# Kernel tuning notes

Hardware: AMD Instinct MI355X
Metric: run time of the kernel (lower is better)

Reference implementation:

```python
import jax, jax.numpy as jnp
import numpy as np

N, E, R, D, S = 50000, 400000, 500, 128, 20
P = R * S
EPS = 1e-5

def setup_inputs() -> dict:
    key = jax.random.key(0)
    ks = jax.random.split(key, 20)
    xav = (2.0 / (D + D)) ** 0.5  # xavier_normal std for square layers
    def W(k):
        return jax.random.normal(k, (D, D), jnp.float32) * xav
    inp = {
        'ent_emb': jax.random.normal(ks[0], (N, D), jnp.float32),
        'rel_emb': jax.random.normal(ks[1], (R, D), jnp.float32),
        'edge_Wo': W(ks[2]), 'edge_bo': jnp.zeros((D,), jnp.float32),
        'edge_Wi': W(ks[3]), 'edge_bi': jnp.zeros((D,), jnp.float32),
        'edge_g': jnp.ones((D,), jnp.float32), 'edge_b': jnp.zeros((D,), jnp.float32),
        'node_Wo': W(ks[4]), 'node_bo': jnp.zeros((D,), jnp.float32),
        'node_Wi': W(ks[5]), 'node_bi': jnp.zeros((D,), jnp.float32),
        'node_g': jnp.ones((D,), jnp.float32), 'node_b': jnp.zeros((D,), jnp.float32),
        'comp_Wo': W(ks[6]), 'comp_bo': jnp.zeros((D,), jnp.float32),
        'comp_Wi': W(ks[7]), 'comp_bi': jnp.zeros((D,), jnp.float32),
        'comp_g': jnp.ones((D,), jnp.float32), 'comp_b': jnp.zeros((D,), jnp.float32),
        'relW': W(ks[8]), 'relb': jnp.zeros((D,), jnp.float32),
        'src': jax.random.randint(ks[9], (E,), 0, N),
        'dst': jax.random.randint(ks[10], (E,), 0, N),
        'etype': jax.random.randint(ks[11], (E,), 0, R),
        'heads': jax.random.randint(ks[13], (P,), 0, N),
        'tails': jax.random.randint(ks[14], (P,), 0, N),
        'rel_ids': jnp.repeat(jnp.arange(R), S),  # S sampled pairs per relation
    }
    in_mask = jax.random.randint(ks[12], (E,), 0, 2).astype(bool)
    inp['in_mask'] = in_mask
    inp['out_mask'] = ~in_mask  # DGL forward/reverse edge split: complementary masks
    return inp

def _edge_softmax(logit, dst, n):
    # segment softmax over edges grouped by destination node
    m = jax.ops.segment_max(logit, dst, num_segments=n)
    e = jnp.exp(logit - m[dst])
    s = jax.ops.segment_sum(e, dst, num_segments=n)
    return e / s[dst]

def _in_out(x, in_m, out_m, Wo, bo, Wi, bi):
    ho = x @ Wo.T + bo
    hi = x @ Wi.T + bi
    h = jnp.where(out_m[:, None], ho, jnp.zeros((), x.dtype))
    return jnp.where(in_m[:, None], hi, h)  # in-edges overwrite (masks disjoint)

def _bn_tanh(x, g, b):
    # training-mode BatchNorm1d (biased batch variance) + Tanh
    mu = jnp.mean(x, 0)
    var = jnp.mean(jnp.square(x - mu), 0)
    return jnp.tanh(g * (x - mu) * jax.lax.rsqrt(var + EPS) + b)

def reference(ent_emb, rel_emb,
              edge_Wo, edge_bo, edge_Wi, edge_bi, edge_g, edge_b,
              node_Wo, node_bo, node_Wi, node_bi, node_g, node_b,
              comp_Wo, comp_bo, comp_Wi, comp_bi, comp_g, comp_b,
              relW, relb,
              src, dst, etype, in_mask, out_mask, heads, tails, rel_ids):
    n = ent_emb.shape[0]
    r = rel_emb.shape[0]
    rel_e = rel_emb[etype]      # [E,D]
    e_src = ent_emb[src]        # [E,D]
    e_dst = ent_emb[dst]        # [E,D]

    # EdgeLayer: attn = e_dot_v(rel_e, dst_emb)
    a = _edge_softmax(jnp.sum(rel_e * e_dst, -1), dst, n)
    h = _in_out(rel_e, in_mask, out_mask, edge_Wo, edge_bo, edge_Wi, edge_bi) * a[:, None]
    edge_ent = _bn_tanh(jax.ops.segment_sum(h, dst, num_segments=n), edge_g, edge_b)

    # NodeLayer: attn = u_dot_v, message = src emb
    a = _edge_softmax(jnp.sum(e_src * e_dst, -1), dst, n)
    h = _in_out(e_src, in_mask, out_mask, node_Wo, node_bo, node_Wi, node_bi) * a[:, None]
    node_ent = _bn_tanh(jax.ops.segment_sum(h, dst, num_segments=n), node_g, node_b)

    # CompLayer (comp_fn='mul'): comp = u_mul_e, attn = e_dot_v(comp, dst)
    comp = e_src * rel_e
    a = _edge_softmax(jnp.sum(comp * e_dst, -1), dst, n)
    h = _in_out(comp, in_mask, out_mask, comp_Wo, comp_bo, comp_Wi, comp_bi) * a[:, None]
    comp_ent = _bn_tanh(jax.ops.segment_sum(h, dst, num_segments=n), comp_g, comp_b)

    final_ent = comp_ent + ent_emb + edge_ent + node_ent

    # update_relations: mean of w_rel_edge(tail - head) per relation
    pair = ent_emb[tails] - ent_emb[heads]          # [P,D]
    upd = pair @ relW.T + relb
    ssum = jax.ops.segment_sum(upd, rel_ids, num_segments=r)
    cnt = jax.ops.segment_sum(jnp.ones((rel_ids.shape[0],), jnp.float32), rel_ids, num_segments=r)
    cnt = jnp.maximum(cnt, 1.0)[:, None]
    final_rel = rel_emb + jnp.tanh(ssum / cnt)
    return final_ent, final_rel
```

## Files before the change

### kernel.cpp

```cpp
#include <hip/hip_runtime.h>
#include <stdint.h>

#define DN 128

typedef short s16x8 __attribute__((ext_vector_type(8)));
typedef float f32x4 __attribute__((ext_vector_type(4)));

__device__ __forceinline__ float bfs(unsigned short u){ return __uint_as_float(((uint32_t)u) << 16); }
__device__ __forceinline__ uint32_t f2bf(float f){
    uint32_t x = __float_as_uint(f);
    return (x + 0x7FFFu + ((x >> 16) & 1u)) >> 16;
}
__device__ __forceinline__ uint32_t packbf(float a, float b){ return f2bf(a) | (f2bf(b) << 16); }
__device__ __forceinline__ float tanh_(float x){
    float e = __expf(2.0f * x);
    return 1.0f - 2.0f / (e + 1.0f);
}

struct WC { const float* src[6]; };
__global__ void k_pre(const int* dst, int* counts,
                      const uint32_t* maskw, int nwords, int* flag,
                      WC wc, unsigned short* wcv, int E){
    int gid = blockIdx.x * 256 + threadIdx.x;
    if (gid < E) atomicAdd(&counts[dst[gid]], 1);
    if (gid < nwords && maskw[gid] > 1u) atomicOr(flag, 1);
    if (gid < 6 * 16384){
        int m = gid >> 14, o = gid & 16383;
        wcv[(size_t)m * 16384 + o] = (unsigned short)f2bf(wc.src[m][o]);
    }
}

__global__ void k_scan_a(const int* counts, int* bsums){
    int t = threadIdx.x;
    int s = counts[blockIdx.x * 256 + t];
    #pragma unroll
    for (int o = 32; o; o >>= 1) s += __shfl_xor(s, o);
    __shared__ int wsum[4];
    if ((t & 63) == 0) wsum[t >> 6] = s;
    __syncthreads();
    if (t == 0) bsums[blockIdx.x] = wsum[0] + wsum[1] + wsum[2] + wsum[3];
}

__global__ void k_scan_bc(const int* counts, const int* bsums, int nsb,
                          int* rowst, int* cursor, int npad, int E){
    __shared__ int pref;
    __shared__ int wsum[4];
    __shared__ int buf[256];
    int t = threadIdx.x, bid = blockIdx.x;
    int s = (t < bid && t < nsb) ? bsums[t] : 0;
    #pragma unroll
    for (int o = 32; o; o >>= 1) s += __shfl_xor(s, o);
    if ((t & 63) == 0) wsum[t >> 6] = s;
    __syncthreads();
    if (t == 0) pref = wsum[0] + wsum[1] + wsum[2] + wsum[3];
    int i = bid * 256 + t;
    int c = counts[i];
    buf[t] = c;
    __syncthreads();
    for (int o = 1; o < 256; o <<= 1){
        int add = (t >= o) ? buf[t - o] : 0;
        __syncthreads();
        buf[t] += add;
        __syncthreads();
    }
    int rsv = buf[t] - c + pref;
    rowst[i] = rsv; cursor[i] = rsv;
    if (i == npad - 1) rowst[npad] = E;
}

__global__ void k_scatter(const int* dst, const int* src, const int* etype,
                          const unsigned char* mask8, const int* flagp,
                          int* cursor, uint32_t* epack, int E){
    int e = blockIdx.x * blockDim.x + threadIdx.x;
    if (e >= E) return;
    int bmode = *flagp;
    int mk = bmode ? (int)mask8[e] : ((const int*)mask8)[e];
    int pos = atomicAdd(&cursor[dst[e]], 1);
    epack[pos] = ((uint32_t)src[e] << 16) | ((uint32_t)etype[e] << 1) | (uint32_t)(mk != 0);
}

__global__ __launch_bounds__(256)
void k_node(const float4* ent4, const float4* rel4,
            const uint32_t* epack, const int* rowst,
            uint32_t* Sw, float* Rv, int Nn, int npad)
{
    int t = threadIdx.x, lane = t & 63, wv = t >> 6;
    int v = blockIdx.x * 4 + wv;
    if (v >= npad) return;
    int sl = lane & 31, half = lane >> 5;

    float4 d4 = {0.f, 0.f, 0.f, 0.f};
    int deg = 0, rs = 0;
    if (v < Nn){
        rs = rowst[v]; deg = rowst[v + 1] - rs;
        d4 = ent4[(size_t)v * 32 + sl];
    }
    float m0 = -1e30f, m1 = -1e30f, m2 = -1e30f;
    float si0 = 0, si1 = 0, si2 = 0, so0 = 0, so1 = 0, so2 = 0;
    float4 aI0 = {0,0,0,0}, aO0 = {0,0,0,0};
    float4 aI1 = {0,0,0,0}, aO1 = {0,0,0,0};
    float4 aI2 = {0,0,0,0}, aO2 = {0,0,0,0};

    for (int base = 0; base < deg; base += 64){
        int nb = min(64, deg - base);
        uint32_t pk = 0;
        if (lane < nb) pk = epack[rs + base + lane];
        int npair = (nb + 1) >> 1;
        for (int j = 0; j < npair; ++j){
            int ei = 2 * j + half;
            uint32_t w = (uint32_t)__shfl((int)pk, ei);
            int sj = (int)(w >> 16);
            int tj = (int)((w >> 1) & 0x7FFF);
            float mk = (float)(w & 1u);
            bool pad = (ei >= nb);
            float4 s4 = ent4[(size_t)sj * 32 + sl];
            float4 r4 = rel4[(size_t)tj * 32 + sl];
            float4 c4 = { s4.x*r4.x, s4.y*r4.y, s4.z*r4.z, s4.w*r4.w };
            float p0 = r4.x*d4.x + r4.y*d4.y + r4.z*d4.z + r4.w*d4.w;
            float p1 = s4.x*d4.x + s4.y*d4.y + s4.z*d4.z + s4.w*d4.w;
            float p2 = c4.x*d4.x + c4.y*d4.y + c4.z*d4.z + c4.w*d4.w;
            #pragma unroll
            for (int o = 1; o < 32; o <<= 1){
                p0 += __shfl_xor(p0, o);
                p1 += __shfl_xor(p1, o);
                p2 += __shfl_xor(p2, o);
            }
            if (pad){ p0 = -1e38f; p1 = -1e38f; p2 = -1e38f; }
            {
                float nm = fmaxf(m0, p0);
                float f = __expf(m0 - nm);
                si0 *= f; so0 *= f;
                aI0.x*=f; aI0.y*=f; aI0.z*=f; aI0.w*=f;
                aO0.x*=f; aO0.y*=f; aO0.z*=f; aO0.w*=f;
                m0 = nm;
                float e = __expf(p0 - m0);
                float ein = e * mk, eout = e - ein;
                si0 += ein; so0 += eout;
                aI0.x += ein*r4.x; aI0.y += ein*r4.y; aI0.z += ein*r4.z; aI0.w += ein*r4.w;
                aO0.x += eout*r4.x; aO0.y += eout*r4.y; aO0.z += eout*r4.z; aO0.w += eout*r4.w;
            }
            {
                float nm = fmaxf(m1, p1);
                float f = __expf(m1 - nm);
                si1 *= f; so1 *= f;
                aI1.x*=f; aI1.y*=f; aI1.z*=f; aI1.w*=f;
                aO1.x*=f; aO1.y*=f; aO1.z*=f; aO1.w*=f;
                m1 = nm;
                float e = __expf(p1 - m1);
                float ein = e * mk, eout = e - ein;
                si1 += ein; so1 += eout;
                aI1.x += ein*s4.x; aI1.y += ein*s4.y; aI1.z += ein*s4.z; aI1.w += ein*s4.w;
                aO1.x += eout*s4.x; aO1.y += eout*s4.y; aO1.z += eout*s4.z; aO1.w += eout*s4.w;
            }
            {
                float nm = fmaxf(m2, p2);
                float f = __expf(m2 - nm);
                si2 *= f; so2 *= f;
                aI2.x*=f; aI2.y*=f; aI2.z*=f; aI2.w*=f;
                aO2.x*=f; aO2.y*=f; aO2.z*=f; aO2.w*=f;
                m2 = nm;
                float e = __expf(p2 - m2);
                float ein = e * mk, eout = e - ein;
                si2 += ein; so2 += eout;
                aI2.x += ein*c4.x; aI2.y += ein*c4.y; aI2.z += ein*c4.z; aI2.w += ein*c4.w;
                aO2.x += eout*c4.x; aO2.y += eout*c4.y; aO2.z += eout*c4.z; aO2.w += eout*c4.w;
            }
        }
    }

    {
        float mo, nm, f;
#define MRG(m, si, so, aI, aO)                                            \
        mo = __shfl_xor(m, 32);                                           \
        nm = fmaxf(m, mo);                                                \
        f = __expf(m - nm);                                               \
        si *= f; so *= f;                                                 \
        aI.x*=f; aI.y*=f; aI.z*=f; aI.w*=f;                               \
        aO.x*=f; aO.y*=f; aO.z*=f; aO.w*=f;                               \
        si += __shfl_xor(si, 32);                                         \
        so += __shfl_xor(so, 32);                                         \
        aI.x += __shfl_xor(aI.x, 32); aI.y += __shfl_xor(aI.y, 32);       \
        aI.z += __shfl_xor(aI.z, 32); aI.w += __shfl_xor(aI.w, 32);       \
        aO.x += __shfl_xor(aO.x, 32); aO.y += __shfl_xor(aO.y, 32);       \
        aO.z += __shfl_xor(aO.z, 32); aO.w += __shfl_xor(aO.w, 32);
        MRG(m0, si0, so0, aI0, aO0)
        MRG(m1, si1, so1, aI1, aO1)
        MRG(m2, si2, so2, aI2, aO2)
#undef MRG
    }

    if (half == 0){
        uint2* S2 = (uint2*)Sw;
        size_t s2 = (size_t)npad * 32;
        size_t wi = (size_t)v * 32 + sl;
        float st, inv;
        st = si0 + so0; inv = st > 0.f ? 1.f / st : 0.f;
        S2[0*s2 + wi] = make_uint2(packbf(aI0.x*inv, aI0.y*inv), packbf(aI0.z*inv, aI0.w*inv));
        S2[1*s2 + wi] = make_uint2(packbf(aO0.x*inv, aO0.y*inv), packbf(aO0.z*inv, aO0.w*inv));
        float ri0 = si0*inv, ro0 = so0*inv;
        st = si1 + so1; inv = st > 0.f ? 1.f / st : 0.f;
        S2[2*s2 + wi] = make_uint2(packbf(aI1.x*inv, aI1.y*inv), packbf(aI1.z*inv, aI1.w*inv));
        S2[3*s2 + wi] = make_uint2(packbf(aO1.x*inv, aO1.y*inv), packbf(aO1.z*inv, aO1.w*inv));
        float ri1 = si1*inv, ro1 = so1*inv;
        st = si2 + so2; inv = st > 0.f ? 1.f / st : 0.f;
        S2[4*s2 + wi] = make_uint2(packbf(aI2.x*inv, aI2.y*inv), packbf(aI2.z*inv, aI2.w*inv));
        S2[5*s2 + wi] = make_uint2(packbf(aO2.x*inv, aO2.y*inv), packbf(aO2.z*inv, aO2.w*inv));
        float ri2 = si2*inv, ro2 = so2*inv;
        if (sl == 0){
            Rv[0*(size_t)npad + v] = ri0; Rv[1*(size_t)npad + v] = ro0;
            Rv[2*(size_t)npad + v] = ri1; Rv[3*(size_t)npad + v] = ro1;
            Rv[4*(size_t)npad + v] = ri2; Rv[5*(size_t)npad + v] = ro2;
        }
    }
}

struct GArgs {
    const short* Wi[3]; const short* Wo[3];
    const float* bi[3]; const float* bo[3];
};

__global__ __launch_bounds__(256)
void k_gemm(GArgs ga, const short* Sb, const float* Rv, unsigned short* P, float* stats,
            int npad, int Nn)
{
    __shared__ float lsum[128], lsq[128];
    int t = threadIdx.x;
    if (t < 128){ lsum[t] = 0.f; lsq[t] = 0.f; }
    __syncthreads();
    int l = blockIdx.y;
    int lane = t & 63, wv = t >> 6;
    int lo = lane & 15, hi = lane >> 4;
    int r0 = blockIdx.x * 64 + wv * 16;
    size_t sstride = (size_t)npad * DN;
    const short* Sin  = Sb + (size_t)(2*l)   * sstride;
    const short* Sout = Sb + (size_t)(2*l+1) * sstride;
    const short* Wi = ga.Wi[l]; const short* Wo = ga.Wo[l];

    s16x8 ain[4], aout[4];
    #pragma unroll
    for (int kb = 0; kb < 4; ++kb){
        size_t o = (size_t)(r0 + lo) * DN + kb*32 + hi*8;
        ain[kb]  = *(const s16x8*)(Sin + o);
        aout[kb] = *(const s16x8*)(Sout + o);
    }
    float rin[4], rout[4];
    const float* RvI = Rv + (size_t)(2*l)   * npad;
    const float* RvO = Rv + (size_t)(2*l+1) * npad;
    #pragma unroll
    for (int rg = 0; rg < 4; ++rg){
        int vr = r0 + hi*4 + rg;
        rin[rg] = RvI[vr]; rout[rg] = RvO[vr];
    }
    unsigned short* Pl = P + (size_t)l * sstride;

    #pragma unroll
    for (int ct = 0; ct < 8; ++ct){
        f32x4 acc = {0.f, 0.f, 0.f, 0.f};
        #pragma unroll
        for (int kb = 0; kb < 4; ++kb){
            size_t wo = (size_t)(ct*16 + lo) * DN + kb*32 + hi*8;
            s16x8 bwi = *(const s16x8*)(Wi + wo);
            acc = __builtin_amdgcn_mfma_f32_16x16x32_bf16(ain[kb], bwi, acc, 0, 0, 0);
            s16x8 bwo = *(const s16x8*)(Wo + wo);
            acc = __builtin_amdgcn_mfma_f32_16x16x32_bf16(aout[kb], bwo, acc, 0, 0, 0);
        }
        int j = ct*16 + lo;
        float biv = ga.bi[l][j], bov = ga.bo[l][j];
        float cs = 0.f, cq = 0.f;
        #pragma unroll
        for (int rg = 0; rg < 4; ++rg){
            float pv = acc[rg] + rin[rg]*biv + rout[rg]*bov;
            Pl[(size_t)(r0 + hi*4 + rg) * DN + j] = (unsigned short)f2bf(pv);
            cs += pv; cq += pv*pv;
        }
        cs += __shfl_xor(cs, 16); cs += __shfl_xor(cs, 32);
        cq += __shfl_xor(cq, 16); cq += __shfl_xor(cq, 32);
        if (lane < 16){ atomicAdd(&lsum[j], cs); atomicAdd(&lsq[j], cq); }
    }
    __syncthreads();
    if (t < 128){
        atomicAdd(&stats[l*128 + t], lsum[t]);
        atomicAdd(&stats[384 + l*128 + t], lsq[t]);
    }
}

struct FArgs { const float* g[3]; const float* b[3]; };

__global__ __launch_bounds__(256)
void k_fin(const unsigned short* Pb, const float* stats, FArgs fa,
           const float* ent, const float* relW, const float* relb,
           const float* rel, const int* heads, const int* tails,
           float* outp, int Nn, int npad, int FB, int Sp)
{
    int t = threadIdx.x, bid = blockIdx.x;
    if (bid < FB){
        __shared__ float sAB[768];
        for (int i = t; i < 384; i += 256){
            int l = i >> 7;
            float su = stats[i], sq = stats[384 + i];
            float mu = su / (float)Nn;
            float var = fmaxf(sq / (float)Nn - mu*mu, 0.f);
            float inv = rsqrtf(var + 1e-5f);
            float g = fa.g[l][i & 127], b = fa.b[l][i & 127];
            sAB[i] = g * inv;
            sAB[384 + i] = b - mu * g * inv;
        }
        __syncthreads();
        int gid = bid * 256 + t;
        if (gid >= Nn * 32) return;
        int v = gid >> 5, q4 = (gid & 31) * 4;
        size_t pst = (size_t)npad * DN;
        size_t pb = (size_t)v * DN + q4;
        ushort4 p0 = *(const ushort4*)(Pb + pb);
        ushort4 p1 = *(const ushort4*)(Pb + pst + pb);
        ushort4 p2 = *(const ushort4*)(Pb + 2*pst + pb);
        float4 e4 = *(const float4*)(ent + (size_t)v * DN + q4);
        float pe[4] = { e4.x, e4.y, e4.z, e4.w };
        unsigned short pu[3][4] = { {p0.x, p0.y, p0.z, p0.w},
                                    {p1.x, p1.y, p1.z, p1.w},
                                    {p2.x, p2.y, p2.z, p2.w} };
        float o[4];
        #pragma unroll
        for (int q = 0; q < 4; ++q){
            float s = pe[q];
            #pragma unroll
            for (int l = 0; l < 3; ++l){
                int jj = l*128 + q4 + q;
                s += tanh_(sAB[jj] * bfs(pu[l][q]) + sAB[384 + jj]);
            }
            o[q] = s;
        }
        float4 ov = { o[0], o[1], o[2], o[3] };
        *(float4*)(outp + (size_t)v * DN + q4) = ov;
    } else {
        __shared__ float mp[256];
        int rr = (bid - FB) * 2 + (t >> 7);
        int j = t & 127;
        float acc = 0.f;
        for (int s = 0; s < Sp; ++s){
            int p = rr * Sp + s;
            acc += ent[(size_t)tails[p] * DN + j] - ent[(size_t)heads[p] * DN + j];
        }
        mp[t] = acc / (float)Sp;
        __syncthreads();
        float dot = relb[j];
        const float4* wr = (const float4*)(relW + (size_t)j * DN);
        const float* mpr = mp + (t >> 7) * 128;
        #pragma unroll 8
        for (int kb = 0; kb < 32; ++kb){
            float4 w = wr[kb];
            dot += mpr[kb*4+0]*w.x + mpr[kb*4+1]*w.y + mpr[kb*4+2]*w.z + mpr[kb*4+3]*w.w;
        }
        outp[(size_t)Nn * DN + (size_t)rr * DN + j] = rel[(size_t)rr * DN + j] + tanh_(dot);
    }
}

extern "C" void kernel_launch(void* const* d_in, const int* in_sizes, int n_in,
                              void* d_out, int out_size, void* d_ws, size_t ws_size,
                              hipStream_t stream)
{
    const float* entf = (const float*)d_in[0];
    const float* relf = (const float*)d_in[1];
    const float* eWo = (const float*)d_in[2];  const float* ebo = (const float*)d_in[3];
    const float* eWi = (const float*)d_in[4];  const float* ebi = (const float*)d_in[5];
    const float* eg  = (const float*)d_in[6];  const float* eb  = (const float*)d_in[7];
    const float* nWo = (const float*)d_in[8];  const float* nbo = (const float*)d_in[9];
    const float* nWi = (const float*)d_in[10]; const float* nbi = (const float*)d_in[11];
    const float* ng  = (const float*)d_in[12]; const float* nb_ = (const float*)d_in[13];
    const float* cWo = (const float*)d_in[14]; const float* cbo = (const float*)d_in[15];
    const float* cWi = (const float*)d_in[16]; const float* cbi = (const float*)d_in[17];
    const float* cg  = (const float*)d_in[18]; const float* cb  = (const float*)d_in[19];
    const float* relWs  = (const float*)d_in[20];
    const float* relb32 = (const float*)d_in[21];
    const int* srcp   = (const int*)d_in[22];
    const int* dstp   = (const int*)d_in[23];
    const int* etyp   = (const int*)d_in[24];
    const int* headsp = (const int*)d_in[25];
    const int* tailsp = (const int*)d_in[26];
    const unsigned char* mask8 = (const unsigned char*)d_in[28];

    int Nn = in_sizes[0] / DN;
    int Rr = in_sizes[1] / DN;
    int E  = in_sizes[22];
    int Pp = in_sizes[25];
    int Sp = Pp / Rr;
    int npad = ((Nn + 255) / 256) * 256;
    int nsb = npad / 256;

    char* w = (char*)d_ws; size_t off = 0;
    auto carve = [&](size_t b) -> void* {
        void* p = w + off; off = (off + b + 255) & ~(size_t)255; return p;
    };
    int*   flag   = (int*)  carve(4);
    int*   counts = (int*)  carve((size_t)npad * 4);
    float* stats  = (float*)carve(1024 * 4);
    size_t zlen = off;
    int*   rowst  = (int*)  carve((size_t)(npad + 1) * 4);
    int*   cursor = (int*)  carve((size_t)npad * 4);
    uint32_t* epack = (uint32_t*)carve((size_t)E * 4);
    int*   bsums  = (int*)  carve(1024 * 4);
    unsigned short* wcv = (unsigned short*)carve((size_t)6 * 16384 * 2);
    short* Sb     = (short*)carve((size_t)6 * npad * DN * 2);
    unsigned short* Pb = (unsigned short*)carve((size_t)3 * npad * DN * 2);
    float* Rv     = (float*)carve((size_t)6 * npad * 4);

    hipMemsetAsync(d_ws, 0, zlen, stream);

    WC wc; wc.src[0] = eWi; wc.src[1] = nWi; wc.src[2] = cWi;
           wc.src[3] = eWo; wc.src[4] = nWo; wc.src[5] = cWo;
    int nwords = 4096;
    k_pre<<<(E + 255) / 256, 256, 0, stream>>>(dstp, counts, (const uint32_t*)mask8,
                                               nwords, flag, wc, wcv, E);
    k_scan_a<<<nsb, 256, 0, stream>>>(counts, bsums);
    k_scan_bc<<<nsb, 256, 0, stream>>>(counts, bsums, nsb, rowst, cursor, npad, E);
    k_scatter<<<(E + 255) / 256, 256, 0, stream>>>(dstp, srcp, etyp, mask8, flag,
                                                   cursor, epack, E);

    k_node<<<npad / 4, 256, 0, stream>>>((const float4*)entf, (const float4*)relf,
                                         epack, rowst, (uint32_t*)Sb, Rv, Nn, npad);

    GArgs ga;
    ga.Wi[0] = (const short*)(wcv + 0*16384);
    ga.Wi[1] = (const short*)(wcv + 1*16384);
    ga.Wi[2] = (const short*)(wcv + 2*16384);
    ga.Wo[0] = (const short*)(wcv + 3*16384);
    ga.Wo[1] = (const short*)(wcv + 4*16384);
    ga.Wo[2] = (const short*)(wcv + 5*16384);
    ga.bi[0] = ebi; ga.bi[1] = nbi; ga.bi[2] = cbi;
    ga.bo[0] = ebo; ga.bo[1] = nbo; ga.bo[2] = cbo;
    k_gemm<<<dim3(npad / 64, 3), 256, 0, stream>>>(ga, Sb, Rv, Pb, stats, npad, Nn);

    FArgs fa;
    fa.g[0] = eg; fa.g[1] = ng; fa.g[2] = cg;
    fa.b[0] = eb; fa.b[1] = nb_; fa.b[2] = cb;
    int FB = (Nn * 32 + 255) / 256;
    int grid = FB + Rr / 2;
    k_fin<<<grid, 256, 0, stream>>>(Pb, stats, fa, entf, relWs, relb32, relf,
                                    headsp, tailsp, (float*)d_out, Nn, npad, FB, Sp);
}
```

Baseline: 393.7 us.

## Spread BN stat atomics over partial buffers and reduce in a separate kernel

The GEMM kernel now spreads its per-block batch-norm sum and sum-of-squares atomics across 64 partial stat buffers chosen by block index, instead of all blocks hitting one 768-float array. A new single-block kernel reduces the partials and computes the BN scale and shift once. The final kernel then just copies those coefficients instead of every block recomputing them. This costs an extra kernel launch and a larger memset, in exchange for less atomic contention and less redundant per-block work.

Measured after the change: 391.9 us. About the same (-0.4%).

```diff
diff --git a/kernel.cpp b/kernel.cpp
--- a/kernel.cpp
+++ b/kernel.cpp
@@ -2,6 +2,7 @@
 #include <stdint.h>
 
 #define DN 128
+#define NSTAT 64
 
 typedef short s16x8 __attribute__((ext_vector_type(8)));
 typedef float f32x4 __attribute__((ext_vector_type(4)));
@@ -220,8 +221,8 @@
 };
 
 __global__ __launch_bounds__(256)
-void k_gemm(GArgs ga, const short* Sb, const float* Rv, unsigned short* P, float* stats,
-            int npad, int Nn)
+void k_gemm(GArgs ga, const short* Sb, const float* Rv, unsigned short* P,
+            float* statsP, int npad, int Nn)
 {
     __shared__ float lsum[128], lsq[128];
     int t = threadIdx.x;
@@ -278,16 +279,34 @@
         if (lane < 16){ atomicAdd(&lsum[j], cs); atomicAdd(&lsq[j], cq); }
     }
     __syncthreads();
+    float* stats = statsP + (size_t)((blockIdx.x ^ (blockIdx.y << 4)) & (NSTAT-1)) * 768;
     if (t < 128){
         atomicAdd(&stats[l*128 + t], lsum[t]);
         atomicAdd(&stats[384 + l*128 + t], lsq[t]);
     }
 }
 
-struct FArgs { const float* g[3]; const float* b[3]; };
+struct BArgs { const float* g[3]; const float* b[3]; };
+
+__global__ void k_bn(BArgs ba, const float* statsP, float* bnAB, int Nn){
+    int t = threadIdx.x;
+    if (t >= 384) return;
+    float su = 0.f, sq = 0.f;
+    for (int k = 0; k < NSTAT; ++k){
+        su += statsP[(size_t)k * 768 + t];
+        sq += statsP[(size_t)k * 768 + 384 + t];
+    }
+    int l = t >> 7;
+    float mu = su / (float)Nn;
+    float var = fmaxf(sq / (float)Nn - mu*mu, 0.f);
+    float inv = rsqrtf(var + 1e-5f);
+    float g = ba.g[l][t & 127], b = ba.b[l][t & 127];
+    bnAB[t] = g * inv;
+    bnAB[384 + t] = b - mu * g * inv;
+}
 
 __global__ __launch_bounds__(256)
-void k_fin(const unsigned short* Pb, const float* stats, FArgs fa,
+void k_fin(const unsigned short* Pb, const float* bnAB,
            const float* ent, const float* relW, const float* relb,
            const float* rel, const int* heads, const int* tails,
            float* outp, int Nn, int npad, int FB, int Sp)
@@ -295,16 +314,7 @@
     int t = threadIdx.x, bid = blockIdx.x;
     if (bid < FB){
         __shared__ float sAB[768];
-        for (int i = t; i < 384; i += 256){
-            int l = i >> 7;
-            float su = stats[i], sq = stats[384 + i];
-            float mu = su / (float)Nn;
-            float var = fmaxf(sq / (float)Nn - mu*mu, 0.f);
-            float inv = rsqrtf(var + 1e-5f);
-            float g = fa.g[l][i & 127], b = fa.b[l][i & 127];
-            sAB[i] = g * inv;
-            sAB[384 + i] = b - mu * g * inv;
-        }
+        for (int i = t; i < 768; i += 256) sAB[i] = bnAB[i];
         __syncthreads();
         int gid = bid * 256 + t;
         if (gid >= Nn * 32) return;
@@ -393,7 +403,7 @@
     };
     int*   flag   = (int*)  carve(4);
     int*   counts = (int*)  carve((size_t)npad * 4);
-    float* stats  = (float*)carve(1024 * 4);
+    float* statsP = (float*)carve((size_t)NSTAT * 768 * 4);
     size_t zlen = off;
     int*   rowst  = (int*)  carve((size_t)(npad + 1) * 4);
     int*   cursor = (int*)  carve((size_t)npad * 4);
@@ -403,6 +413,7 @@
     short* Sb     = (short*)carve((size_t)6 * npad * DN * 2);
     unsigned short* Pb = (unsigned short*)carve((size_t)3 * npad * DN * 2);
     float* Rv     = (float*)carve((size_t)6 * npad * 4);
+    float* bnAB   = (float*)carve(768 * 4);
 
     hipMemsetAsync(d_ws, 0, zlen, stream);
 
@@ -428,13 +439,15 @@
     ga.Wo[2] = (const short*)(wcv + 5*16384);
     ga.bi[0] = ebi; ga.bi[1] = nbi; ga.bi[2] = cbi;
     ga.bo[0] = ebo; ga.bo[1] = nbo; ga.bo[2] = cbo;
-    k_gemm<<<dim3(npad / 64, 3), 256, 0, stream>>>(ga, Sb, Rv, Pb, stats, npad, Nn);
-
-    FArgs fa;
-    fa.g[0] = eg; fa.g[1] = ng; fa.g[2] = cg;
-    fa.b[0] = eb; fa.b[1] = nb_; fa.b[2] = cb;
+    k_gemm<<<dim3(npad / 64, 3), 256, 0, stream>>>(ga, Sb, Rv, Pb, statsP, npad, Nn);
+
+    BArgs ba;
+    ba.g[0] = eg; ba.g[1] = ng; ba.g[2] = cg;
+    ba.b[0] = eb; ba.b[1] = nb_; ba.b[2] = cb;
+    k_bn<<<1, 384, 0, stream>>>(ba, statsP, bnAB, Nn);
+
     int FB = (Nn * 32 + 255) / 256;
     int grid = FB + Rr / 2;
-    k_fin<<<grid, 256, 0, stream>>>(Pb, stats, fa, entf, relWs, relb32, relf,
+    k_fin<<<grid, 256, 0, stream>>>(Pb, bnAB, entf, relWs, relb32, relf,
                                     headsp, tailsp, (float*)d_out, Nn, npad, FB, Sp);
 }
```
